# Kernel tuning notes

Measured on AMD Instinct MI355X. Metric: run time of the kernel, lower is better.

## Reference

```python
import jax, jax.numpy as jnp
import numpy as np

DIM, DEPTH, MULT = 512, 3, 4
E = 2 ** DEPTH            # 8 experts
HID = MULT * DIM          # 2048
B, S = 4, 1024


def setup_inputs() -> dict:
    key = jax.random.key(0)
    ks = jax.random.split(key, 7)
    sd = 1.0 / np.sqrt(DIM)
    sh = 1.0 / np.sqrt(HID)
    return {
        "x": jax.random.normal(ks[0], (B, S, DIM), dtype=jnp.float32),
        "rw": jax.random.normal(ks[1], (E - 1, DIM), dtype=jnp.float32) * sd,
        "rb": jax.random.normal(ks[2], (E - 1,), dtype=jnp.float32) * sd,
        "w1": jax.random.normal(ks[3], (E, DIM, HID), dtype=jnp.float32) * sd,
        "b1": jax.random.normal(ks[4], (E, HID), dtype=jnp.float32) * sd,
        "w2": jax.random.normal(ks[5], (E, HID, DIM), dtype=jnp.float32) * sh,
        "b2": jax.random.normal(ks[6], (E, DIM), dtype=jnp.float32) * sh,
    }


def _leaf_probs(flat_x, rw, rb):
    # Binary-tree soft routing: level d has 2**d routers at offset 2**d - 1.
    n_tok = flat_x.shape[0]
    leaf = jnp.ones((n_tok, 1), dtype=flat_x.dtype)
    for d in range(DEPTH):
        off, n = 2 ** d - 1, 2 ** d
        logits = flat_x @ rw[off:off + n].T + rb[off:off + n]   # [N, n]
        p = jax.nn.sigmoid(logits)
        # child probs: left = 1-p, right = p
        leaf = (leaf[:, :, None] * jnp.stack([1.0 - p, p], axis=2)).reshape(n_tok, 2 * n)
    return leaf  # [N, E]


def reference(x, rw, rb, w1, b1, w2, b2):
    b, s, dim = x.shape
    flat_x = x.reshape(b * s, dim)                               # [N, D]
    leaf_probs = _leaf_probs(flat_x, rw, rb)                     # [N, E]
    # Dense evaluation of all experts (soft-routing training path).
    h = jnp.einsum('nd,edh->neh', flat_x, w1) + b1[None]         # [N, E, H]
    h = jax.nn.gelu(h, approximate=False)                        # torch nn.GELU (erf)
    y = jnp.einsum('neh,ehd->ned', h, w2) + b2[None]             # [N, E, D]
    out = jnp.einsum('ned,ne->nd', y, leaf_probs)                # [N, D]
    return out.reshape(b, s, dim)
```

## Files before the change

### kernel.cpp

```cpp
#include <hip/hip_runtime.h>
#include <hip/hip_bf16.h>
#include <hip/hip_fp16.h>

#define DIM 512
#define HID 2048
#define NE 8
#define NTOK 4096

typedef _Float16 v8h __attribute__((ext_vector_type(8)));
typedef _Float16 v4h __attribute__((ext_vector_type(4)));
typedef float v4f __attribute__((ext_vector_type(4)));

__device__ __forceinline__ void load16(const void* g, void* l) {
  __builtin_amdgcn_global_load_lds(
      (const __attribute__((address_space(1))) unsigned int*)g,
      (__attribute__((address_space(3))) unsigned int*)l, 16, 0, 0);
}

__device__ __forceinline__ float gelu_erf(float v) {
  float z = v * 0.70710678118654752f;
  float az = __builtin_fabsf(z);
  float t = __builtin_amdgcn_rcpf(1.0f + 0.3275911f * az);
  float poly = 1.061405429f;
  poly = poly * t - 1.453152027f;
  poly = poly * t + 1.421413741f;
  poly = poly * t - 0.284496736f;
  poly = poly * t + 0.254829592f;
  poly = poly * t;
  float erf_abs = 1.0f - poly * __expf(-z * z);
  float erf = __builtin_copysignf(erf_abs, z);
  return 0.5f * v * (1.0f + erf);
}

__global__ __launch_bounds__(256) void convert_x_kernel(const float* __restrict__ x,
                                                        _Float16* __restrict__ xh) {
  size_t i = ((size_t)blockIdx.x * 256 + threadIdx.x) * 8;
  const float4* xv = (const float4*)(x + i);
  float4 a = xv[0], b = xv[1];
  v8h o;
  o[0] = (_Float16)a.x; o[1] = (_Float16)a.y; o[2] = (_Float16)a.z; o[3] = (_Float16)a.w;
  o[4] = (_Float16)b.x; o[5] = (_Float16)b.y; o[6] = (_Float16)b.z; o[7] = (_Float16)b.w;
  *(v8h*)(xh + i) = o;
}

__global__ __launch_bounds__(256) void transpose_cvt_kernel(const float* __restrict__ in,
                                                            _Float16* __restrict__ outp,
                                                            int R, int C, int tiles_r,
                                                            int blocks_per_e) {
  const int bx = blockIdx.x;
  const int e = bx / blocks_per_e;
  const int rem = bx - e * blocks_per_e;
  const int rt = rem % tiles_r;
  const int ct = rem / tiles_r;
  const int r0 = rt << 5, c0 = ct << 5;
  __shared__ float tile[32][33];
  const int tr = threadIdx.x >> 3;
  const int tc = (threadIdx.x & 7) << 2;
  const float4 v = *(const float4*)(in + (size_t)e * R * C + (size_t)(r0 + tr) * C + c0 + tc);
  tile[tc + 0][tr] = v.x;
  tile[tc + 1][tr] = v.y;
  tile[tc + 2][tr] = v.z;
  tile[tc + 3][tr] = v.w;
  __syncthreads();
  v4h h;
  h[0] = (_Float16)tile[tr][tc + 0];
  h[1] = (_Float16)tile[tr][tc + 1];
  h[2] = (_Float16)tile[tr][tc + 2];
  h[3] = (_Float16)tile[tr][tc + 3];
  *(v4h*)(outp + (size_t)e * R * C + (size_t)(c0 + tr) * R + r0 + tc) = h;
}

__global__ __launch_bounds__(256) void routing_kernel(const float* __restrict__ x,
                                                      const float* __restrict__ rw,
                                                      const float* __restrict__ rb,
                                                      float* __restrict__ leaf) {
  const int lane = threadIdx.x & 63;
  const int wave = threadIdx.x >> 6;
  const int n = (blockIdx.x << 2) + wave;
  const float4* xv = (const float4*)(x + (size_t)n * DIM);
  const float4 x0 = xv[lane * 2], x1 = xv[lane * 2 + 1];
  float logits[7];
#pragma unroll
  for (int rr = 0; rr < 7; ++rr) {
    const float4* wv = (const float4*)(rw + rr * DIM);
    const float4 w0 = wv[lane * 2], w1v = wv[lane * 2 + 1];
    float s = x0.x * w0.x + x0.y * w0.y + x0.z * w0.z + x0.w * w0.w +
              x1.x * w1v.x + x1.y * w1v.y + x1.z * w1v.z + x1.w * w1v.w;
#pragma unroll
    for (int o = 32; o; o >>= 1) s += __shfl_xor(s, o, 64);
    logits[rr] = s + rb[rr];
  }
  if (lane < NE) {
    const int eidx = lane;
    const float p0 = 1.f / (1.f + __expf(-logits[0]));
    float f = ((eidx >> 2) & 1) ? p0 : 1.f - p0;
    const float p1 = 1.f / (1.f + __expf(-logits[1 + (eidx >> 2)]));
    f *= ((eidx >> 1) & 1) ? p1 : 1.f - p1;
    const float p2 = 1.f / (1.f + __expf(-logits[3 + (eidx >> 1)]));
    f *= (eidx & 1) ? p2 : 1.f - p2;
    leaf[(size_t)n * NE + eidx] = f;
  }
}

__global__ __launch_bounds__(256) void gemm1_kernel(const _Float16* __restrict__ xh,
                                                    const _Float16* __restrict__ w1t,
                                                    const float* __restrict__ b1,
                                                    _Float16* __restrict__ H,
                                                    int e_base, int ecnt) {
  const int bx = blockIdx.x;
  const int e_local = bx % ecnt;
  const int t = bx / ecnt;
  const int mt = t & 31;
  const int nt = t >> 5;
  const int e = e_base + e_local;
  const int m0 = mt << 7, n0 = nt << 7;

  __shared__ alignas(16) _Float16 As[128 * 64];
  __shared__ alignas(16) _Float16 Bs[128 * 64];

  const int tid = threadIdx.x;
  const int lane = tid & 63;
  const int wave = tid >> 6;
  const int qm = wave >> 1, qn = wave & 1;
  const int r = lane & 15, q = lane >> 4;

  const _Float16* Ab = xh + (size_t)m0 * DIM;
  const _Float16* Bb = w1t + ((size_t)e * HID + n0) * DIM;

  v4f acc[4][4];
#pragma unroll
  for (int i = 0; i < 4; ++i)
#pragma unroll
    for (int j = 0; j < 4; ++j) acc[i][j] = v4f{0.f, 0.f, 0.f, 0.f};

  const int ch0 = wave << 8;
  for (int k0 = 0; k0 < DIM; k0 += 64) {
#pragma unroll
    for (int i = 0; i < 4; ++i) {
      const int ch = ch0 + (i << 6) + lane;
      const int row = ch >> 3, c8 = ch & 7;
      load16(Ab + (size_t)row * DIM + k0 + (c8 << 3), As + (size_t)ch * 8);
      load16(Bb + (size_t)row * DIM + k0 + (c8 << 3), Bs + (size_t)ch * 8);
    }
    __syncthreads();
#pragma unroll
    for (int ks = 0; ks < 64; ks += 32) {
      v8h a[4], b[4];
#pragma unroll
      for (int i = 0; i < 4; ++i)
        a[i] = *(const v8h*)(As + ((qm << 6) + (i << 4) + r) * 64 + ks + (q << 3));
#pragma unroll
      for (int j = 0; j < 4; ++j)
        b[j] = *(const v8h*)(Bs + ((qn << 6) + (j << 4) + r) * 64 + ks + (q << 3));
#pragma unroll
      for (int i = 0; i < 4; ++i)
#pragma unroll
        for (int j = 0; j < 4; ++j)
          acc[i][j] = __builtin_amdgcn_mfma_f32_16x16x32_f16(a[i], b[j], acc[i][j], 0, 0, 0);
    }
    __syncthreads();
  }

  const float* b1e = b1 + (size_t)e * HID;
  _Float16* He = H + (size_t)e_local * NTOK * HID;
#pragma unroll
  for (int j = 0; j < 4; ++j) {
    const int col = n0 + (qn << 6) + (j << 4) + r;
    const float bias = b1e[col];
#pragma unroll
    for (int i = 0; i < 4; ++i) {
      const int rowb = m0 + (qm << 6) + (i << 4) + (q << 2);
#pragma unroll
      for (int rr = 0; rr < 4; ++rr) {
        float v = acc[i][j][rr] + bias;
        He[(size_t)(rowb + rr) * HID + col] = (_Float16)gelu_erf(v);
      }
    }
  }
}

__global__ __launch_bounds__(256) void gemm2_kernel(const _Float16* __restrict__ H,
                                                    const _Float16* __restrict__ w2t,
                                                    const float* __restrict__ b2,
                                                    const float* __restrict__ leaf,
                                                    float* __restrict__ out,
                                                    int e_base, int ecnt) {
  const int bx = blockIdx.x;
  const int e_local = bx % ecnt;
  const int t = bx / ecnt;
  const int mt = t & 31;
  const int dt = t >> 5;
  const int e = e_base + e_local;
  const int m0 = mt << 7, d0 = dt << 7;

  __shared__ alignas(16) _Float16 As[128 * 64];
  __shared__ alignas(16) _Float16 Bs[128 * 64];

  const int tid = threadIdx.x;
  const int lane = tid & 63;
  const int wave = tid >> 6;
  const int qm = wave >> 1, qn = wave & 1;
  const int r = lane & 15, q = lane >> 4;

  const _Float16* Ab = H + ((size_t)e_local * NTOK + m0) * HID;
  const _Float16* Bb = w2t + ((size_t)e * DIM + d0) * HID;

  v4f acc[4][4];
#pragma unroll
  for (int i = 0; i < 4; ++i)
#pragma unroll
    for (int j = 0; j < 4; ++j) acc[i][j] = v4f{0.f, 0.f, 0.f, 0.f};

  const int ch0 = wave << 8;
  for (int k0 = 0; k0 < HID; k0 += 64) {
#pragma unroll
    for (int i = 0; i < 4; ++i) {
      const int ch = ch0 + (i << 6) + lane;
      const int row = ch >> 3, c8 = ch & 7;
      load16(Ab + (size_t)row * HID + k0 + (c8 << 3), As + (size_t)ch * 8);
      load16(Bb + (size_t)row * HID + k0 + (c8 << 3), Bs + (size_t)ch * 8);
    }
    __syncthreads();
#pragma unroll
    for (int ks = 0; ks < 64; ks += 32) {
      v8h a[4], b[4];
#pragma unroll
      for (int i = 0; i < 4; ++i)
        a[i] = *(const v8h*)(As + ((qm << 6) + (i << 4) + r) * 64 + ks + (q << 3));
#pragma unroll
      for (int j = 0; j < 4; ++j)
        b[j] = *(const v8h*)(Bs + ((qn << 6) + (j << 4) + r) * 64 + ks + (q << 3));
#pragma unroll
      for (int i = 0; i < 4; ++i)
#pragma unroll
        for (int j = 0; j < 4; ++j)
          acc[i][j] = __builtin_amdgcn_mfma_f32_16x16x32_f16(a[i], b[j], acc[i][j], 0, 0, 0);
    }
    __syncthreads();
  }

  const float* b2e = b2 + (size_t)e * DIM;
#pragma unroll
  for (int i = 0; i < 4; ++i) {
    const int rowb = m0 + (qm << 6) + (i << 4) + (q << 2);
    float p[4];
#pragma unroll
    for (int rr = 0; rr < 4; ++rr) p[rr] = leaf[(size_t)(rowb + rr) * NE + e];
#pragma unroll
    for (int j = 0; j < 4; ++j) {
      const int col = d0 + (qn << 6) + (j << 4) + r;
      const float bias = b2e[col];
#pragma unroll
      for (int rr = 0; rr < 4; ++rr) {
        atomicAdd(out + (size_t)(rowb + rr) * DIM + col, p[rr] * (acc[i][j][rr] + bias));
      }
    }
  }
}

extern "C" void kernel_launch(void* const* d_in, const int* in_sizes, int n_in,
                              void* d_out, int out_size, void* d_ws, size_t ws_size,
                              hipStream_t stream) {
  const float* x  = (const float*)d_in[0];
  const float* rw = (const float*)d_in[1];
  const float* rb = (const float*)d_in[2];
  const float* w1 = (const float*)d_in[3];
  const float* b1 = (const float*)d_in[4];
  const float* w2 = (const float*)d_in[5];
  const float* b2 = (const float*)d_in[6];
  float* out = (float*)d_out;

  char* ws = (char*)d_ws;
  const size_t xh_bytes  = (size_t)NTOK * DIM * 2;
  const size_t w1t_bytes = (size_t)NE * HID * DIM * 2;
  const size_t w2t_bytes = (size_t)NE * DIM * HID * 2;
  const size_t leaf_bytes = (size_t)NTOK * NE * 4;
  _Float16* xh   = (_Float16*)(ws);
  _Float16* w1t  = (_Float16*)(ws + xh_bytes);
  _Float16* w2t  = (_Float16*)(ws + xh_bytes + w1t_bytes);
  float*    leaf = (float*)(ws + xh_bytes + w1t_bytes + w2t_bytes);
  _Float16* Hbuf = (_Float16*)(ws + xh_bytes + w1t_bytes + w2t_bytes + leaf_bytes);
  const size_t used = xh_bytes + w1t_bytes + w2t_bytes + leaf_bytes;
  const size_t Hper = (size_t)NTOK * HID * 2;

  int EC = 1;
  if (ws_size >= used + 8 * Hper) EC = 8;
  else if (ws_size >= used + 4 * Hper) EC = 4;
  else if (ws_size >= used + 2 * Hper) EC = 2;
  if (ws_size < used + Hper) return;

  hipMemsetAsync(d_out, 0, (size_t)out_size * sizeof(float), stream);
  convert_x_kernel<<<1024, 256, 0, stream>>>(x, xh);
  transpose_cvt_kernel<<<8192, 256, 0, stream>>>(w1, w1t, DIM, HID, DIM / 32, 1024);
  transpose_cvt_kernel<<<8192, 256, 0, stream>>>(w2, w2t, HID, DIM, HID / 32, 1024);
  routing_kernel<<<1024, 256, 0, stream>>>(x, rw, rb, leaf);
  for (int e0 = 0; e0 < NE; e0 += EC) {
    gemm1_kernel<<<EC * 512, 256, 0, stream>>>(xh, w1t, b1, Hbuf, e0, EC);
    gemm2_kernel<<<EC * 128, 256, 0, stream>>>(Hbuf, w2t, b2, leaf, out, e0, EC);
  }
}
```

Baseline: 400.7 us.

## Fold routing probs into H, split-K gemm2 across experts, swizzle LDS, fuse prep kernels

Routing now also writes the fp16 copy of x, and the two weight transposes are merged into one kernel that uses 64x32 tiles and 16-byte stores. A new out_init kernel writes the probability-weighted b2 sum, replacing the memset. gemm1 scales GELU(h) by the leaf probability, so gemm2 can contract over experts and hidden units together: it runs as a 4-way split-K over 8*2048 with atomics, and no longer needs per-expert bias or prob handling. Both GEMMs also XOR-swizzle their LDS layout to cut bank conflicts. This needs the full 8-expert H buffer in workspace and returns early if it is too small. Storing H pre-scaled in fp16 changes rounding.

```diff
diff --git a/kernel.cpp b/kernel.cpp
--- a/kernel.cpp
+++ b/kernel.cpp
@@ -8,7 +8,6 @@
 #define NTOK 4096
 
 typedef _Float16 v8h __attribute__((ext_vector_type(8)));
-typedef _Float16 v4h __attribute__((ext_vector_type(4)));
 typedef float v4f __attribute__((ext_vector_type(4)));
 
 __device__ __forceinline__ void load16(const void* g, void* l) {
@@ -32,53 +31,20 @@
   return 0.5f * v * (1.0f + erf);
 }
 
-__global__ __launch_bounds__(256) void convert_x_kernel(const float* __restrict__ x,
-                                                        _Float16* __restrict__ xh) {
-  size_t i = ((size_t)blockIdx.x * 256 + threadIdx.x) * 8;
-  const float4* xv = (const float4*)(x + i);
-  float4 a = xv[0], b = xv[1];
-  v8h o;
-  o[0] = (_Float16)a.x; o[1] = (_Float16)a.y; o[2] = (_Float16)a.z; o[3] = (_Float16)a.w;
-  o[4] = (_Float16)b.x; o[5] = (_Float16)b.y; o[6] = (_Float16)b.z; o[7] = (_Float16)b.w;
-  *(v8h*)(xh + i) = o;
-}
-
-__global__ __launch_bounds__(256) void transpose_cvt_kernel(const float* __restrict__ in,
-                                                            _Float16* __restrict__ outp,
-                                                            int R, int C, int tiles_r,
-                                                            int blocks_per_e) {
-  const int bx = blockIdx.x;
-  const int e = bx / blocks_per_e;
-  const int rem = bx - e * blocks_per_e;
-  const int rt = rem % tiles_r;
-  const int ct = rem / tiles_r;
-  const int r0 = rt << 5, c0 = ct << 5;
-  __shared__ float tile[32][33];
-  const int tr = threadIdx.x >> 3;
-  const int tc = (threadIdx.x & 7) << 2;
-  const float4 v = *(const float4*)(in + (size_t)e * R * C + (size_t)(r0 + tr) * C + c0 + tc);
-  tile[tc + 0][tr] = v.x;
-  tile[tc + 1][tr] = v.y;
-  tile[tc + 2][tr] = v.z;
-  tile[tc + 3][tr] = v.w;
-  __syncthreads();
-  v4h h;
-  h[0] = (_Float16)tile[tr][tc + 0];
-  h[1] = (_Float16)tile[tr][tc + 1];
-  h[2] = (_Float16)tile[tr][tc + 2];
-  h[3] = (_Float16)tile[tr][tc + 3];
-  *(v4h*)(outp + (size_t)e * R * C + (size_t)(c0 + tr) * R + r0 + tc) = h;
-}
-
 __global__ __launch_bounds__(256) void routing_kernel(const float* __restrict__ x,
                                                       const float* __restrict__ rw,
                                                       const float* __restrict__ rb,
-                                                      float* __restrict__ leaf) {
+                                                      float* __restrict__ leaf,
+                                                      _Float16* __restrict__ xh) {
   const int lane = threadIdx.x & 63;
   const int wave = threadIdx.x >> 6;
   const int n = (blockIdx.x << 2) + wave;
   const float4* xv = (const float4*)(x + (size_t)n * DIM);
   const float4 x0 = xv[lane * 2], x1 = xv[lane * 2 + 1];
+  v8h o;
+  o[0] = (_Float16)x0.x; o[1] = (_Float16)x0.y; o[2] = (_Float16)x0.z; o[3] = (_Float16)x0.w;
+  o[4] = (_Float16)x1.x; o[5] = (_Float16)x1.y; o[6] = (_Float16)x1.z; o[7] = (_Float16)x1.w;
+  *(v8h*)(xh + (size_t)n * DIM + lane * 8) = o;
   float logits[7];
 #pragma unroll
   for (int rr = 0; rr < 7; ++rr) {
@@ -87,7 +53,7 @@
     float s = x0.x * w0.x + x0.y * w0.y + x0.z * w0.z + x0.w * w0.w +
               x1.x * w1v.x + x1.y * w1v.y + x1.z * w1v.z + x1.w * w1v.w;
 #pragma unroll
-    for (int o = 32; o; o >>= 1) s += __shfl_xor(s, o, 64);
+    for (int o2 = 32; o2; o2 >>= 1) s += __shfl_xor(s, o2, 64);
     logits[rr] = s + rb[rr];
   }
   if (lane < NE) {
@@ -102,17 +68,70 @@
   }
 }
 
+__global__ __launch_bounds__(256) void transpose_cvt2_kernel(const float* __restrict__ w1,
+                                                             _Float16* __restrict__ w1t,
+                                                             const float* __restrict__ w2,
+                                                             _Float16* __restrict__ w2t) {
+  int bx = blockIdx.x;
+  const float* in;
+  _Float16* outp;
+  int R, C;
+  if (bx < 4096) { in = w1; outp = w1t; R = DIM; C = HID; }
+  else { bx -= 4096; in = w2; outp = w2t; R = HID; C = DIM; }
+  const int e = bx >> 9;
+  const int rem = bx & 511;
+  const int tiles_r = R >> 6;
+  const int rt = rem % tiles_r;
+  const int ct = rem / tiles_r;
+  const int r0 = rt << 6, c0 = ct << 5;
+  const size_t ebase = (size_t)e * R * C;
+
+  __shared__ float tile[32][65];
+  const int tid = threadIdx.x;
+#pragma unroll
+  for (int it = 0; it < 2; ++it) {
+    const int s = tid + (it << 8);
+    const int row = s >> 3, cq = s & 7;
+    const float4 v = *(const float4*)(in + ebase + (size_t)(r0 + row) * C + c0 + (cq << 2));
+    tile[(cq << 2) + 0][row] = v.x;
+    tile[(cq << 2) + 1][row] = v.y;
+    tile[(cq << 2) + 2][row] = v.z;
+    tile[(cq << 2) + 3][row] = v.w;
+  }
+  __syncthreads();
+  const int c = tid >> 3, seg = tid & 7;
+  v8h h;
+#pragma unroll
+  for (int u = 0; u < 8; ++u) h[u] = (_Float16)tile[c][(seg << 3) + u];
+  *(v8h*)(outp + ebase + (size_t)(c0 + c) * R + r0 + (seg << 3)) = h;
+}
+
+__global__ __launch_bounds__(256) void out_init_kernel(const float* __restrict__ leaf,
+                                                       const float* __restrict__ b2,
+                                                       float* __restrict__ out) {
+  const int g = blockIdx.x * 256 + threadIdx.x;
+  const int n = g >> 7, dq = g & 127;
+  const float* lp = leaf + (size_t)n * NE;
+  float4 acc = {0.f, 0.f, 0.f, 0.f};
+#pragma unroll
+  for (int e = 0; e < NE; ++e) {
+    const float pe = lp[e];
+    const float4 bv = *(const float4*)(b2 + (size_t)e * DIM + (dq << 2));
+    acc.x += pe * bv.x; acc.y += pe * bv.y; acc.z += pe * bv.z; acc.w += pe * bv.w;
+  }
+  *(float4*)(out + (size_t)n * DIM + (dq << 2)) = acc;
+}
+
 __global__ __launch_bounds__(256) void gemm1_kernel(const _Float16* __restrict__ xh,
                                                     const _Float16* __restrict__ w1t,
                                                     const float* __restrict__ b1,
-                                                    _Float16* __restrict__ H,
-                                                    int e_base, int ecnt) {
+                                                    const float* __restrict__ leaf,
+                                                    _Float16* __restrict__ H) {
   const int bx = blockIdx.x;
-  const int e_local = bx % ecnt;
-  const int t = bx / ecnt;
+  const int e = bx & 7;
+  const int t = bx >> 3;
   const int mt = t & 31;
   const int nt = t >> 5;
-  const int e = e_base + e_local;
   const int m0 = mt << 7, n0 = nt << 7;
 
   __shared__ alignas(16) _Float16 As[128 * 64];
@@ -138,7 +157,8 @@
 #pragma unroll
     for (int i = 0; i < 4; ++i) {
       const int ch = ch0 + (i << 6) + lane;
-      const int row = ch >> 3, c8 = ch & 7;
+      const int row = ch >> 3;
+      const int c8 = (ch & 7) ^ (row & 7);
       load16(Ab + (size_t)row * DIM + k0 + (c8 << 3), As + (size_t)ch * 8);
       load16(Bb + (size_t)row * DIM + k0 + (c8 << 3), Bs + (size_t)ch * 8);
     }
@@ -147,11 +167,17 @@
     for (int ks = 0; ks < 64; ks += 32) {
       v8h a[4], b[4];
 #pragma unroll
-      for (int i = 0; i < 4; ++i)
-        a[i] = *(const v8h*)(As + ((qm << 6) + (i << 4) + r) * 64 + ks + (q << 3));
-#pragma unroll
-      for (int j = 0; j < 4; ++j)
-        b[j] = *(const v8h*)(Bs + ((qn << 6) + (j << 4) + r) * 64 + ks + (q << 3));
+      for (int i = 0; i < 4; ++i) {
+        const int row = (qm << 6) + (i << 4) + r;
+        const int s = (((ks >> 3) + q) ^ (row & 7));
+        a[i] = *(const v8h*)(As + (row << 6) + (s << 3));
+      }
+#pragma unroll
+      for (int j = 0; j < 4; ++j) {
+        const int row = (qn << 6) + (j << 4) + r;
+        const int s = (((ks >> 3) + q) ^ (row & 7));
+        b[j] = *(const v8h*)(Bs + (row << 6) + (s << 3));
+      }
 #pragma unroll
       for (int i = 0; i < 4; ++i)
 #pragma unroll
@@ -162,18 +188,21 @@
   }
 
   const float* b1e = b1 + (size_t)e * HID;
-  _Float16* He = H + (size_t)e_local * NTOK * HID;
-#pragma unroll
-  for (int j = 0; j < 4; ++j) {
-    const int col = n0 + (qn << 6) + (j << 4) + r;
-    const float bias = b1e[col];
-#pragma unroll
-    for (int i = 0; i < 4; ++i) {
-      const int rowb = m0 + (qm << 6) + (i << 4) + (q << 2);
-#pragma unroll
-      for (int rr = 0; rr < 4; ++rr) {
-        float v = acc[i][j][rr] + bias;
-        He[(size_t)(rowb + rr) * HID + col] = (_Float16)gelu_erf(v);
+  _Float16* He = H + (size_t)e * NTOK * HID;
+  float bias[4];
+#pragma unroll
+  for (int j = 0; j < 4; ++j) bias[j] = b1e[n0 + (qn << 6) + (j << 4) + r];
+#pragma unroll
+  for (int i = 0; i < 4; ++i) {
+    const int rowb = m0 + (qm << 6) + (i << 4) + (q << 2);
+#pragma unroll
+    for (int rr = 0; rr < 4; ++rr) {
+      const int row = rowb + rr;
+      const float p = leaf[(size_t)row * NE + e];
+#pragma unroll
+      for (int j = 0; j < 4; ++j) {
+        const int col = n0 + (qn << 6) + (j << 4) + r;
+        He[(size_t)row * HID + col] = (_Float16)(p * gelu_erf(acc[i][j][rr] + bias[j]));
       }
     }
   }
@@ -181,17 +210,13 @@
 
 __global__ __launch_bounds__(256) void gemm2_kernel(const _Float16* __restrict__ H,
                                                     const _Float16* __restrict__ w2t,
-                                                    const float* __restrict__ b2,
-                                                    const float* __restrict__ leaf,
-                                                    float* __restrict__ out,
-                                                    int e_base, int ecnt) {
+                                                    float* __restrict__ out) {
   const int bx = blockIdx.x;
-  const int e_local = bx % ecnt;
-  const int t = bx / ecnt;
-  const int mt = t & 31;
-  const int dt = t >> 5;
-  const int e = e_base + e_local;
+  const int mt = bx & 31;
+  const int dt = (bx >> 5) & 3;
+  const int sp = bx >> 7;
   const int m0 = mt << 7, d0 = dt << 7;
+  const int kbase = sp << 12;
 
   __shared__ alignas(16) _Float16 As[128 * 64];
   __shared__ alignas(16) _Float16 Bs[128 * 64];
@@ -202,9 +227,6 @@
   const int qm = wave >> 1, qn = wave & 1;
   const int r = lane & 15, q = lane >> 4;
 
-  const _Float16* Ab = H + ((size_t)e_local * NTOK + m0) * HID;
-  const _Float16* Bb = w2t + ((size_t)e * DIM + d0) * HID;
-
   v4f acc[4][4];
 #pragma unroll
   for (int i = 0; i < 4; ++i)
@@ -212,24 +234,36 @@
     for (int j = 0; j < 4; ++j) acc[i][j] = v4f{0.f, 0.f, 0.f, 0.f};
 
   const int ch0 = wave << 8;
-  for (int k0 = 0; k0 < HID; k0 += 64) {
+  for (int kk = 0; kk < 4096; kk += 64) {
+    const int kg = kbase + kk;
+    const int e = kg >> 11;
+    const int kl = kg & 2047;
+    const _Float16* Ab = H + ((size_t)e * NTOK + m0) * HID + kl;
+    const _Float16* Bb = w2t + ((size_t)e * DIM + d0) * HID + kl;
 #pragma unroll
     for (int i = 0; i < 4; ++i) {
       const int ch = ch0 + (i << 6) + lane;
-      const int row = ch >> 3, c8 = ch & 7;
-      load16(Ab + (size_t)row * HID + k0 + (c8 << 3), As + (size_t)ch * 8);
-      load16(Bb + (size_t)row * HID + k0 + (c8 << 3), Bs + (size_t)ch * 8);
+      const int row = ch >> 3;
+      const int c8 = (ch & 7) ^ (row & 7);
+      load16(Ab + (size_t)row * HID + (c8 << 3), As + (size_t)ch * 8);
+      load16(Bb + (size_t)row * HID + (c8 << 3), Bs + (size_t)ch * 8);
     }
     __syncthreads();
 #pragma unroll
     for (int ks = 0; ks < 64; ks += 32) {
       v8h a[4], b[4];
 #pragma unroll
-      for (int i = 0; i < 4; ++i)
-        a[i] = *(const v8h*)(As + ((qm << 6) + (i << 4) + r) * 64 + ks + (q << 3));
-#pragma unroll
-      for (int j = 0; j < 4; ++j)
-        b[j] = *(const v8h*)(Bs + ((qn << 6) + (j << 4) + r) * 64 + ks + (q << 3));
+      for (int i = 0; i < 4; ++i) {
+        const int row = (qm << 6) + (i << 4) + r;
+        const int s = (((ks >> 3) + q) ^ (row & 7));
+        a[i] = *(const v8h*)(As + (row << 6) + (s << 3));
+      }
+#pragma unroll
+      for (int j = 0; j < 4; ++j) {
+        const int row = (qn << 6) + (j << 4) + r;
+        const int s = (((ks >> 3) + q) ^ (row & 7));
+        b[j] = *(const v8h*)(Bs + (row << 6) + (s << 3));
+      }
 #pragma unroll
       for (int i = 0; i < 4; ++i)
 #pragma unroll
@@ -239,21 +273,15 @@
     __syncthreads();
   }
 
-  const float* b2e = b2 + (size_t)e * DIM;
 #pragma unroll
   for (int i = 0; i < 4; ++i) {
     const int rowb = m0 + (qm << 6) + (i << 4) + (q << 2);
-    float p[4];
-#pragma unroll
-    for (int rr = 0; rr < 4; ++rr) p[rr] = leaf[(size_t)(rowb + rr) * NE + e];
 #pragma unroll
     for (int j = 0; j < 4; ++j) {
       const int col = d0 + (qn << 6) + (j << 4) + r;
-      const float bias = b2e[col];
-#pragma unroll
-      for (int rr = 0; rr < 4; ++rr) {
-        atomicAdd(out + (size_t)(rowb + rr) * DIM + col, p[rr] * (acc[i][j][rr] + bias));
-      }
+#pragma unroll
+      for (int rr = 0; rr < 4; ++rr)
+        atomicAdd(out + (size_t)(rowb + rr) * DIM + col, acc[i][j][rr]);
     }
   }
 }
@@ -271,31 +299,21 @@
   float* out = (float*)d_out;
 
   char* ws = (char*)d_ws;
-  const size_t xh_bytes  = (size_t)NTOK * DIM * 2;
-  const size_t w1t_bytes = (size_t)NE * HID * DIM * 2;
-  const size_t w2t_bytes = (size_t)NE * DIM * HID * 2;
+  const size_t xh_bytes   = (size_t)NTOK * DIM * 2;
+  const size_t w1t_bytes  = (size_t)NE * HID * DIM * 2;
+  const size_t w2t_bytes  = (size_t)NE * DIM * HID * 2;
   const size_t leaf_bytes = (size_t)NTOK * NE * 4;
+  const size_t H_bytes    = (size_t)NE * NTOK * HID * 2;
   _Float16* xh   = (_Float16*)(ws);
   _Float16* w1t  = (_Float16*)(ws + xh_bytes);
   _Float16* w2t  = (_Float16*)(ws + xh_bytes + w1t_bytes);
   float*    leaf = (float*)(ws + xh_bytes + w1t_bytes + w2t_bytes);
   _Float16* Hbuf = (_Float16*)(ws + xh_bytes + w1t_bytes + w2t_bytes + leaf_bytes);
-  const size_t used = xh_bytes + w1t_bytes + w2t_bytes + leaf_bytes;
-  const size_t Hper = (size_t)NTOK * HID * 2;
-
-  int EC = 1;
-  if (ws_size >= used + 8 * Hper) EC = 8;
-  else if (ws_size >= used + 4 * Hper) EC = 4;
-  else if (ws_size >= used + 2 * Hper) EC = 2;
-  if (ws_size < used + Hper) return;
-
-  hipMemsetAsync(d_out, 0, (size_t)out_size * sizeof(float), stream);
-  convert_x_kernel<<<1024, 256, 0, stream>>>(x, xh);
-  transpose_cvt_kernel<<<8192, 256, 0, stream>>>(w1, w1t, DIM, HID, DIM / 32, 1024);
-  transpose_cvt_kernel<<<8192, 256, 0, stream>>>(w2, w2t, HID, DIM, HID / 32, 1024);
-  routing_kernel<<<1024, 256, 0, stream>>>(x, rw, rb, leaf);
-  for (int e0 = 0; e0 < NE; e0 += EC) {
-    gemm1_kernel<<<EC * 512, 256, 0, stream>>>(xh, w1t, b1, Hbuf, e0, EC);
-    gemm2_kernel<<<EC * 128, 256, 0, stream>>>(Hbuf, w2t, b2, leaf, out, e0, EC);
-  }
-}
+  if (ws_size < xh_bytes + w1t_bytes + w2t_bytes + leaf_bytes + H_bytes) return;
+
+  routing_kernel<<<1024, 256, 0, stream>>>(x, rw, rb, leaf, xh);
+  transpose_cvt2_kernel<<<8192, 256, 0, stream>>>(w1, w1t, w2, w2t);
+  out_init_kernel<<<2048, 256, 0, stream>>>(leaf, b2, out);
+  gemm1_kernel<<<4096, 256, 0, stream>>>(xh, w1t, b1, leaf, Hbuf);
+  gemm2_kernel<<<512, 256, 0, stream>>>(Hbuf, w2t, out);
+}
```

After: 340.0 us. 15.2% less time.
